# Kernel optimization log

Measured on AMD Instinct MI355X. Metric: run time of the kernel, lower is better.

The kernel has to match this reference:

```python
import jax, jax.numpy as jnp
import numpy as np

PERI_IDX = np.array([0, 1, 2, 3, 5, 6, 7, 8])  # non-center taps of the 3x3 window


def _extract_patches(x, stride, padding):
    # x: [B,C,H,W] -> patches [B,C,9,Hout,Wout], tap k = di*3+dj (row-major), matching F.unfold.
    B, C, H, W = x.shape
    Hout = (H + 2 * padding - 3) // stride + 1
    Wout = (W + 2 * padding - 3) // stride + 1
    xp = jnp.pad(x, ((0, 0), (0, 0), (padding, padding), (padding, padding)))
    taps = [xp[:, :, di:di + (Hout - 1) * stride + 1:stride, dj:dj + (Wout - 1) * stride + 1:stride]
            for di in range(3) for dj in range(3)]
    return jnp.stack(taps, axis=2)  # [B,C,9,Hout,Wout]


def setup_inputs() -> dict:
    key = jax.random.key(0)
    k1, k2, k3, k4 = jax.random.split(key, 4)
    B, C, O, H, W = 8, 64, 64, 128, 128
    x = jax.random.normal(k1, (B, C, H, W), dtype=jnp.float32)
    core = jax.random.normal(k2, (O, C, 1, 1), dtype=jnp.float32) * (1.0 / np.sqrt(C))
    periphery = jax.random.uniform(k3, (8,), dtype=jnp.float32, minval=-0.1, maxval=0.1)
    threshold = jnp.array([0.1], dtype=jnp.float32)
    scale = jnp.array([10.0], dtype=jnp.float32)
    return {"x": x, "core": core, "periphery": periphery, "threshold": threshold,
            "scale": scale, "stride": 1, "padding": 1}


def reference(x, core, periphery, threshold, scale, stride, padding):
    B, C, H, W = x.shape
    O = core.shape[0]
    patches = _extract_patches(x, stride, padding)           # [B,C,9,Ho,Wo]
    center = patches[:, :, 4]                                 # [B,C,Ho,Wo]
    # per-pixel variance-like routing statistic over channels and taps
    div = jnp.sum((patches - center[:, :, None]) ** 2, axis=(1, 2))  # [B,Ho,Wo]
    m_hard = jax.nn.sigmoid((div - threshold[0]) * scale[0]) > 0.5   # [B,Ho,Wo] bool
    w = core.reshape(O, C)
    # path 0 (low variance): 1x1 conv on the center pixel
    zero_out = jnp.einsum('bchw,oc->bohw', center, w)
    # path 1 (high variance): periphery-weighted sum then 1x1 conv
    agg = jnp.einsum('bckhw,k->bchw', patches[:, :, PERI_IDX], periphery)
    one_out = jnp.einsum('bchw,oc->bohw', agg, w)
    return jnp.where(m_hard[:, None], one_out, zero_out)
```

## Files before the change

### kernel.cpp

```cpp
#include <hip/hip_runtime.h>
#include <hip/hip_bf16.h>

constexpr int Bc = 8;
constexpr int Cc = 64;
constexpr int Oc = 64;
constexpr int Hc = 128;
constexpr int Wc = 128;
constexpr int HWc = Hc * Wc;
constexpr int CP = 72;

typedef __attribute__((ext_vector_type(8))) short short8;
typedef __attribute__((ext_vector_type(4))) float floatx4;

__global__ __launch_bounds__(512) void spconv_kernel(
    const float* __restrict__ x, const float* __restrict__ core,
    const float* __restrict__ peri, const float* __restrict__ thr,
    const float* __restrict__ scl, float* __restrict__ out)
{
    __shared__ __hip_bfloat16 s_selT[Wc][CP];
    __shared__ __hip_bfloat16 s_core[Oc][CP];
    __shared__ float s_divp[4][Wc];
    __shared__ float s_msk[Wc];

    const int tid = threadIdx.x;
    const int w   = tid & (Wc - 1);
    const int q   = tid >> 7;
    const int b   = blockIdx.x >> 7;
    const int h   = blockIdx.x & (Hc - 1);

    #pragma unroll
    for (int i = 0; i < 8; ++i) {
        const int idx = i * 512 + tid;
        s_core[idx >> 6][idx & 63] = __float2bfloat16(core[idx]);
    }

    const float* xb = x + (size_t)b * Cc * HWc + (size_t)h * Wc;

    const int   dh[8] = {-1,-1,-1, 0, 0, 1, 1, 1};
    const int   dw[8] = {-1, 0, 1,-1, 1,-1, 0, 1};
    int   off[8];
    float pl[8], mf[8];
    #pragma unroll
    for (int k = 0; k < 8; ++k) {
        const bool okh = (h + dh[k] >= 0) && (h + dh[k] < Hc);
        const bool okw = (w + dw[k] >= 0) && (w + dw[k] < Wc);
        const bool ok  = okh && okw;
        off[k] = ok ? (w + dh[k] * Wc + dw[k]) : w;
        mf[k]  = ok ? 1.f : 0.f;
        pl[k]  = ok ? peri[k] : 0.f;
    }

    float divacc = 0.f;
    const float* rowq = xb + (size_t)(q * 16) * HWc;
    #pragma unroll 4
    for (int ci = 0; ci < 16; ++ci) {
        const float* row = rowq + (size_t)ci * HWc;
        const float t4 = row[w];
        float v[8];
        #pragma unroll
        for (int k = 0; k < 8; ++k) v[k] = row[off[k]];
        float agg = 0.f;
        #pragma unroll
        for (int k = 0; k < 8; ++k) agg = fmaf(pl[k], v[k], agg);
        s_selT[w][q * 16 + ci] = __float2bfloat16(agg);
        #pragma unroll
        for (int k = 0; k < 8; ++k) {
            const float d = fmaf(mf[k], v[k], -t4);
            divacc = fmaf(d, d, divacc);
        }
    }
    s_divp[q][w] = divacc;
    __syncthreads();

    if (tid < Wc) {
        const float div = s_divp[0][tid] + s_divp[1][tid]
                        + s_divp[2][tid] + s_divp[3][tid];
        s_msk[tid] = (((div - thr[0]) * scl[0]) > 0.f) ? 1.f : 0.f;
    }
    __syncthreads();

    #pragma unroll
    for (int i = 0; i < 16; ++i) {
        const int idx = i * 512 + tid;
        const int ww  = idx & (Wc - 1);
        const int c   = idx >> 7;
        if (s_msk[ww] == 0.f)
            s_selT[ww][c] = __float2bfloat16(xb[(size_t)c * HWc + ww]);
    }
    __syncthreads();

    const int lane = tid & 63;
    const int wid  = tid >> 6;
    const int o0   = (wid & 3) * 16;
    const int wh   = wid >> 2;
    const int n    = lane & 15;
    const int quad = lane >> 4;

    const short8 a0 = *(const short8*)&s_core[o0 + n][quad * 8];
    const short8 a1 = *(const short8*)&s_core[o0 + n][quad * 8 + 32];

    float* outb = out + ((size_t)(b * Oc) * Hc + h) * Wc;

    #pragma unroll
    for (int t = 0; t < 4; ++t) {
        const int w0 = (wh * 4 + t) * 16;
        const short8 b0 = *(const short8*)&s_selT[w0 + n][quad * 8];
        const short8 b1 = *(const short8*)&s_selT[w0 + n][quad * 8 + 32];
        floatx4 acc = {0.f, 0.f, 0.f, 0.f};
        acc = __builtin_amdgcn_mfma_f32_16x16x32_bf16(a0, b0, acc, 0, 0, 0);
        acc = __builtin_amdgcn_mfma_f32_16x16x32_bf16(a1, b1, acc, 0, 0, 0);
        #pragma unroll
        for (int r = 0; r < 4; ++r) {
            const int o = o0 + quad * 4 + r;
            outb[(size_t)o * HWc + w0 + n] = acc[r];
        }
    }
}

extern "C" void kernel_launch(void* const* d_in, const int* in_sizes, int n_in,
                              void* d_out, int out_size, void* d_ws, size_t ws_size,
                              hipStream_t stream) {
    const float* x    = (const float*)d_in[0];
    const float* core = (const float*)d_in[1];
    const float* peri = (const float*)d_in[2];
    const float* thr  = (const float*)d_in[3];
    const float* scl  = (const float*)d_in[4];
    float* out = (float*)d_out;

    spconv_kernel<<<dim3(Bc * Hc), dim3(512), 0, stream>>>(
        x, core, peri, thr, scl, out);
}
```

Measured before the change: 106.4 us.

## Register-tile stencil with 4-wide pixel vectors and reorder blocks batch-inner

```diff
diff --git a/kernel.cpp b/kernel.cpp
--- a/kernel.cpp
+++ b/kernel.cpp
@@ -19,14 +19,13 @@
 {
     __shared__ __hip_bfloat16 s_selT[Wc][CP];
     __shared__ __hip_bfloat16 s_core[Oc][CP];
-    __shared__ float s_divp[4][Wc];
+    __shared__ float s_divp[16][132];
     __shared__ float s_msk[Wc];
 
     const int tid = threadIdx.x;
-    const int w   = tid & (Wc - 1);
-    const int q   = tid >> 7;
-    const int b   = blockIdx.x >> 7;
-    const int h   = blockIdx.x & (Hc - 1);
+    const int blk = blockIdx.x;
+    const int b   = blk & 7;
+    const int h   = blk >> 3;
 
     #pragma unroll
     for (int i = 0; i < 8; ++i) {
@@ -34,47 +33,81 @@
         s_core[idx >> 6][idx & 63] = __float2bfloat16(core[idx]);
     }
 
+    const int cg = tid & 15;
+    const int s  = tid >> 4;
+    const int w0 = s * 4;
+    const int c0 = cg * 4;
+
     const float* xb = x + (size_t)b * Cc * HWc + (size_t)h * Wc;
 
-    const int   dh[8] = {-1,-1,-1, 0, 0, 1, 1, 1};
-    const int   dw[8] = {-1, 0, 1,-1, 1,-1, 0, 1};
-    int   off[8];
-    float pl[8], mf[8];
+    const float mU = (h > 0)      ? 1.f : 0.f;
+    const float mD = (h < Hc - 1) ? 1.f : 0.f;
+    const int   dU = (h > 0)      ? -Wc : 0;
+    const int   dD = (h < Hc - 1) ?  Wc : 0;
+    const float mL = (s > 0)  ? 1.f : 0.f;
+    const float mR = (s < 31) ? 1.f : 0.f;
+    const int   oL = (s > 0)  ? (w0 - 1) : w0;
+    const int   oR = (s < 31) ? (w0 + 4) : (w0 + 3);
+    const float mUL = mU * mL, mUR = mU * mR;
+    const float mDL = mD * mL, mDR = mD * mR;
+
+    const float p0 = peri[0], p1 = peri[1], p2 = peri[2], p3 = peri[3];
+    const float p4 = peri[4], p5 = peri[5], p6 = peri[6], p7 = peri[7];
+
+    float dv[4] = {0.f, 0.f, 0.f, 0.f};
+
     #pragma unroll
-    for (int k = 0; k < 8; ++k) {
-        const bool okh = (h + dh[k] >= 0) && (h + dh[k] < Hc);
-        const bool okw = (w + dw[k] >= 0) && (w + dw[k] < Wc);
-        const bool ok  = okh && okw;
-        off[k] = ok ? (w + dh[k] * Wc + dw[k]) : w;
-        mf[k]  = ok ? 1.f : 0.f;
-        pl[k]  = ok ? peri[k] : 0.f;
-    }
+    for (int ci = 0; ci < 4; ++ci) {
+        const float* rc = xb + (size_t)(c0 + ci) * HWc;
+        const float* ru = rc + dU;
+        const float* rd = rc + dD;
 
-    float divacc = 0.f;
-    const float* rowq = xb + (size_t)(q * 16) * HWc;
-    #pragma unroll 4
-    for (int ci = 0; ci < 16; ++ci) {
-        const float* row = rowq + (size_t)ci * HWc;
-        const float t4 = row[w];
-        float v[8];
+        const floatx4 c4 = *(const floatx4*)(rc + w0);
+        const floatx4 u4 = *(const floatx4*)(ru + w0);
+        const floatx4 d4 = *(const floatx4*)(rd + w0);
+
+        float U[6]  = { ru[oL] * mUL, u4[0] * mU, u4[1] * mU,
+                        u4[2] * mU,   u4[3] * mU, ru[oR] * mUR };
+        float Cv[6] = { rc[oL] * mL,  c4[0], c4[1],
+                        c4[2],        c4[3], rc[oR] * mR };
+        float D[6]  = { rd[oL] * mDL, d4[0] * mD, d4[1] * mD,
+                        d4[2] * mD,   d4[3] * mD, rd[oR] * mDR };
+
         #pragma unroll
-        for (int k = 0; k < 8; ++k) v[k] = row[off[k]];
-        float agg = 0.f;
-        #pragma unroll
-        for (int k = 0; k < 8; ++k) agg = fmaf(pl[k], v[k], agg);
-        s_selT[w][q * 16 + ci] = __float2bfloat16(agg);
-        #pragma unroll
-        for (int k = 0; k < 8; ++k) {
-            const float d = fmaf(mf[k], v[k], -t4);
-            divacc = fmaf(d, d, divacc);
+        for (int j = 0; j < 4; ++j) {
+            const float t = Cv[j + 1];
+            float agg =      p0 * U[j];
+            agg = fmaf(p1, U[j + 1],  agg);
+            agg = fmaf(p2, U[j + 2],  agg);
+            agg = fmaf(p3, Cv[j],     agg);
+            agg = fmaf(p4, Cv[j + 2], agg);
+            agg = fmaf(p5, D[j],      agg);
+            agg = fmaf(p6, D[j + 1],  agg);
+            agg = fmaf(p7, D[j + 2],  agg);
+            s_selT[w0 + j][c0 + ci] = __float2bfloat16(agg);
+
+            float e, dd;
+            e = U[j] - t;      dd = e * e;
+            e = U[j + 1] - t;  dd = fmaf(e, e, dd);
+            e = U[j + 2] - t;  dd = fmaf(e, e, dd);
+            e = Cv[j] - t;     dd = fmaf(e, e, dd);
+            e = Cv[j + 2] - t; dd = fmaf(e, e, dd);
+            e = D[j] - t;      dd = fmaf(e, e, dd);
+            e = D[j + 1] - t;  dd = fmaf(e, e, dd);
+            e = D[j + 2] - t;  dd = fmaf(e, e, dd);
+            dv[j] += dd;
         }
     }
-    s_divp[q][w] = divacc;
+    {
+        floatx4 dvv = { dv[0], dv[1], dv[2], dv[3] };
+        *(floatx4*)&s_divp[cg][w0] = dvv;
+    }
     __syncthreads();
 
     if (tid < Wc) {
-        const float div = s_divp[0][tid] + s_divp[1][tid]
-                        + s_divp[2][tid] + s_divp[3][tid];
+        float div = 0.f;
+        #pragma unroll
+        for (int g = 0; g < 16; ++g) div += s_divp[g][tid];
         s_msk[tid] = (((div - thr[0]) * scl[0]) > 0.f) ? 1.f : 0.f;
     }
     __syncthreads();
@@ -103,16 +136,16 @@
 
     #pragma unroll
     for (int t = 0; t < 4; ++t) {
-        const int w0 = (wh * 4 + t) * 16;
-        const short8 b0 = *(const short8*)&s_selT[w0 + n][quad * 8];
-        const short8 b1 = *(const short8*)&s_selT[w0 + n][quad * 8 + 32];
+        const int wt0 = (wh * 4 + t) * 16;
+        const short8 b0 = *(const short8*)&s_selT[wt0 + n][quad * 8];
+        const short8 b1 = *(const short8*)&s_selT[wt0 + n][quad * 8 + 32];
         floatx4 acc = {0.f, 0.f, 0.f, 0.f};
         acc = __builtin_amdgcn_mfma_f32_16x16x32_bf16(a0, b0, acc, 0, 0, 0);
         acc = __builtin_amdgcn_mfma_f32_16x16x32_bf16(a1, b1, acc, 0, 0, 0);
         #pragma unroll
         for (int r = 0; r < 4; ++r) {
             const int o = o0 + quad * 4 + r;
-            outb[(size_t)o * HWc + w0 + n] = acc[r];
+            outb[(size_t)o * HWc + wt0 + n] = acc[r];
         }
     }
 }
```

New measurement: 126.1 us. 18.5% more time.

## Build MFMA operands directly in registers, dropping shared memory and block barriers

Applied to the files above, without the earlier changes.

```diff
diff --git a/kernel.cpp b/kernel.cpp
--- a/kernel.cpp
+++ b/kernel.cpp
@@ -7,112 +7,133 @@
 constexpr int Hc = 128;
 constexpr int Wc = 128;
 constexpr int HWc = Hc * Wc;
-constexpr int CP = 72;
 
 typedef __attribute__((ext_vector_type(8))) short short8;
 typedef __attribute__((ext_vector_type(4))) float floatx4;
+typedef __attribute__((ext_vector_type(2))) float floatx2;
+typedef __attribute__((ext_vector_type(4))) unsigned uintx4;
 
-__global__ __launch_bounds__(512) void spconv_kernel(
+__device__ __forceinline__ unsigned cvt_pk_bf16(float lo, float hi) {
+    unsigned r;
+    asm("v_cvt_pk_bf16_f32 %0, %1, %2" : "=v"(r) : "v"(lo), "v"(hi));
+    return r;
+}
+
+__global__ __launch_bounds__(256, 4) void spconv_kernel(
     const float* __restrict__ x, const float* __restrict__ core,
     const float* __restrict__ peri, const float* __restrict__ thr,
     const float* __restrict__ scl, float* __restrict__ out)
 {
-    __shared__ __hip_bfloat16 s_selT[Wc][CP];
-    __shared__ __hip_bfloat16 s_core[Oc][CP];
-    __shared__ float s_divp[4][Wc];
-    __shared__ float s_msk[Wc];
+    const int tid  = threadIdx.x;
+    const int l    = tid & 63;
+    const int wv   = tid >> 6;
+    const int b    = blockIdx.x & 7;
+    const int rh   = blockIdx.x >> 3;
+    const int h    = rh >> 1;
+    const int half = rh & 1;
+    const int n    = l & 15;
+    const int quad = l >> 4;
+    const int w0   = half * 64 + wv * 16;
+    const int wpix = w0 + n;
 
-    const int tid = threadIdx.x;
-    const int w   = tid & (Wc - 1);
-    const int q   = tid >> 7;
-    const int b   = blockIdx.x >> 7;
-    const int h   = blockIdx.x & (Hc - 1);
+    const int  w2 = wpix & ~1;
+    const bool ep = (wpix & 1) != 0;
+    const bool lm = wpix > 0;
+    const bool rm = wpix < Wc - 1;
+    const int  eoff = ep ? (rm ? wpix + 1 : wpix) : (lm ? wpix - 1 : 0);
 
+    const float mUf = (h > 0) ? 1.f : 0.f;
+    const float mDf = (h < Hc - 1) ? 1.f : 0.f;
+    const int   dU  = (h > 0) ? -Wc : 0;
+    const int   dD  = (h < Hc - 1) ? Wc : 0;
+
+    const float p0 = peri[0], p1 = peri[1], p2 = peri[2], p3 = peri[3];
+    const float p4 = peri[4], p5 = peri[5], p6 = peri[6], p7 = peri[7];
+    const float thrv = thr[0], sclv = scl[0];
+
+    const float* rp0 = x + (size_t)b * Cc * HWc + (size_t)h * Wc;
+
+    float dacc = 0.f;
+    unsigned aggPk[8], cenPk[8];
+
+#define PROCC(CIDX, AGGV, CENV) do {                                          \
+    const float* rp = rp0 + (size_t)(CIDX) * HWc;                             \
+    const floatx2 vU = *(const floatx2*)(rp + dU + w2);                       \
+    const floatx2 vC = *(const floatx2*)(rp + w2);                            \
+    const floatx2 vD = *(const floatx2*)(rp + dD + w2);                       \
+    const float eU = rp[dU + eoff];                                           \
+    const float eC = rp[eoff];                                                \
+    const float eD = rp[dD + eoff];                                           \
+    const float uL = (ep ? vU.x : (lm ? eU : 0.f)) * mUf;                     \
+    const float uC = (ep ? vU.y : vU.x) * mUf;                                \
+    const float uR = (ep ? (rm ? eU : 0.f) : vU.y) * mUf;                     \
+    const float cL =  ep ? vC.x : (lm ? eC : 0.f);                            \
+    const float t  =  ep ? vC.y : vC.x;                                       \
+    const float cR =  ep ? (rm ? eC : 0.f) : vC.y;                            \
+    const float dL = (ep ? vD.x : (lm ? eD : 0.f)) * mDf;                     \
+    const float dC = (ep ? vD.y : vD.x) * mDf;                                \
+    const float dR = (ep ? (rm ? eD : 0.f) : vD.y) * mDf;                     \
+    float a = p0 * uL; a = fmaf(p1, uC, a); a = fmaf(p2, uR, a);              \
+    a = fmaf(p3, cL, a); a = fmaf(p4, cR, a);                                 \
+    a = fmaf(p5, dL, a); a = fmaf(p6, dC, a); a = fmaf(p7, dR, a);            \
+    AGGV = a; CENV = t;                                                       \
+    float e;                                                                  \
+    e = uL - t; dacc = fmaf(e, e, dacc); e = uC - t; dacc = fmaf(e, e, dacc); \
+    e = uR - t; dacc = fmaf(e, e, dacc); e = cL - t; dacc = fmaf(e, e, dacc); \
+    e = cR - t; dacc = fmaf(e, e, dacc); e = dL - t; dacc = fmaf(e, e, dacc); \
+    e = dC - t; dacc = fmaf(e, e, dacc); e = dR - t; dacc = fmaf(e, e, dacc); \
+} while (0)
+
+    const int cb = quad * 8;
     #pragma unroll
-    for (int i = 0; i < 8; ++i) {
-        const int idx = i * 512 + tid;
-        s_core[idx >> 6][idx & 63] = __float2bfloat16(core[idx]);
+    for (int hf = 0; hf < 2; ++hf) {
+        const int cbase = hf * 32 + cb;
+        #pragma unroll
+        for (int jp = 0; jp < 4; ++jp) {
+            float a0, c0v, a1, c1v;
+            PROCC(cbase + 2 * jp,     a0, c0v);
+            PROCC(cbase + 2 * jp + 1, a1, c1v);
+            aggPk[hf * 4 + jp] = cvt_pk_bf16(a0, a1);
+            cenPk[hf * 4 + jp] = cvt_pk_bf16(c0v, c1v);
+        }
+    }
+#undef PROCC
+
+    dacc += __shfl_xor(dacc, 16);
+    dacc += __shfl_xor(dacc, 32);
+    const bool one = ((dacc - thrv) * sclv) > 0.f;
+
+    union { unsigned u[4]; short8 s; } B0, B1;
+    #pragma unroll
+    for (int i = 0; i < 4; ++i) {
+        B0.u[i] = one ? aggPk[i]     : cenPk[i];
+        B1.u[i] = one ? aggPk[i + 4] : cenPk[i + 4];
     }
 
-    const float* xb = x + (size_t)b * Cc * HWc + (size_t)h * Wc;
-
-    const int   dh[8] = {-1,-1,-1, 0, 0, 1, 1, 1};
-    const int   dw[8] = {-1, 0, 1,-1, 1,-1, 0, 1};
-    int   off[8];
-    float pl[8], mf[8];
+    union { unsigned u[4]; short8 s; } A0[4], A1[4];
     #pragma unroll
-    for (int k = 0; k < 8; ++k) {
-        const bool okh = (h + dh[k] >= 0) && (h + dh[k] < Hc);
-        const bool okw = (w + dw[k] >= 0) && (w + dw[k] < Wc);
-        const bool ok  = okh && okw;
-        off[k] = ok ? (w + dh[k] * Wc + dw[k]) : w;
-        mf[k]  = ok ? 1.f : 0.f;
-        pl[k]  = ok ? peri[k] : 0.f;
+    for (int ot = 0; ot < 4; ++ot) {
+        const float* ar = core + (size_t)(ot * 16 + n) * Cc + cb;
+        const floatx4 f0 = *(const floatx4*)(ar);
+        const floatx4 f1 = *(const floatx4*)(ar + 4);
+        const floatx4 f2 = *(const floatx4*)(ar + 32);
+        const floatx4 f3 = *(const floatx4*)(ar + 36);
+        A0[ot].u[0] = cvt_pk_bf16(f0.x, f0.y); A0[ot].u[1] = cvt_pk_bf16(f0.z, f0.w);
+        A0[ot].u[2] = cvt_pk_bf16(f1.x, f1.y); A0[ot].u[3] = cvt_pk_bf16(f1.z, f1.w);
+        A1[ot].u[0] = cvt_pk_bf16(f2.x, f2.y); A1[ot].u[1] = cvt_pk_bf16(f2.z, f2.w);
+        A1[ot].u[2] = cvt_pk_bf16(f3.x, f3.y); A1[ot].u[3] = cvt_pk_bf16(f3.z, f3.w);
     }
 
-    float divacc = 0.f;
-    const float* rowq = xb + (size_t)(q * 16) * HWc;
-    #pragma unroll 4
-    for (int ci = 0; ci < 16; ++ci) {
-        const float* row = rowq + (size_t)ci * HWc;
-        const float t4 = row[w];
-        float v[8];
-        #pragma unroll
-        for (int k = 0; k < 8; ++k) v[k] = row[off[k]];
-        float agg = 0.f;
-        #pragma unroll
-        for (int k = 0; k < 8; ++k) agg = fmaf(pl[k], v[k], agg);
-        s_selT[w][q * 16 + ci] = __float2bfloat16(agg);
-        #pragma unroll
-        for (int k = 0; k < 8; ++k) {
-            const float d = fmaf(mf[k], v[k], -t4);
-            divacc = fmaf(d, d, divacc);
-        }
-    }
-    s_divp[q][w] = divacc;
-    __syncthreads();
-
-    if (tid < Wc) {
-        const float div = s_divp[0][tid] + s_divp[1][tid]
-                        + s_divp[2][tid] + s_divp[3][tid];
-        s_msk[tid] = (((div - thr[0]) * scl[0]) > 0.f) ? 1.f : 0.f;
-    }
-    __syncthreads();
-
+    float* outb = out + (size_t)b * Oc * HWc + (size_t)h * Wc + wpix;
     #pragma unroll
-    for (int i = 0; i < 16; ++i) {
-        const int idx = i * 512 + tid;
-        const int ww  = idx & (Wc - 1);
-        const int c   = idx >> 7;
-        if (s_msk[ww] == 0.f)
-            s_selT[ww][c] = __float2bfloat16(xb[(size_t)c * HWc + ww]);
-    }
-    __syncthreads();
-
-    const int lane = tid & 63;
-    const int wid  = tid >> 6;
-    const int o0   = (wid & 3) * 16;
-    const int wh   = wid >> 2;
-    const int n    = lane & 15;
-    const int quad = lane >> 4;
-
-    const short8 a0 = *(const short8*)&s_core[o0 + n][quad * 8];
-    const short8 a1 = *(const short8*)&s_core[o0 + n][quad * 8 + 32];
-
-    float* outb = out + ((size_t)(b * Oc) * Hc + h) * Wc;
-
-    #pragma unroll
-    for (int t = 0; t < 4; ++t) {
-        const int w0 = (wh * 4 + t) * 16;
-        const short8 b0 = *(const short8*)&s_selT[w0 + n][quad * 8];
-        const short8 b1 = *(const short8*)&s_selT[w0 + n][quad * 8 + 32];
+    for (int ot = 0; ot < 4; ++ot) {
         floatx4 acc = {0.f, 0.f, 0.f, 0.f};
-        acc = __builtin_amdgcn_mfma_f32_16x16x32_bf16(a0, b0, acc, 0, 0, 0);
-        acc = __builtin_amdgcn_mfma_f32_16x16x32_bf16(a1, b1, acc, 0, 0, 0);
+        acc = __builtin_amdgcn_mfma_f32_16x16x32_bf16(A0[ot].s, B0.s, acc, 0, 0, 0);
+        acc = __builtin_amdgcn_mfma_f32_16x16x32_bf16(A1[ot].s, B1.s, acc, 0, 0, 0);
         #pragma unroll
         for (int r = 0; r < 4; ++r) {
-            const int o = o0 + quad * 4 + r;
-            outb[(size_t)o * HWc + w0 + n] = acc[r];
+            const int o = ot * 16 + quad * 4 + r;
+            outb[(size_t)o * HWc] = acc[r];
         }
     }
 }
@@ -127,6 +148,6 @@
     const float* scl  = (const float*)d_in[4];
     float* out = (float*)d_out;
 
-    spconv_kernel<<<dim3(Bc * Hc), dim3(512), 0, stream>>>(
+    spconv_kernel<<<dim3(Bc * Hc * 2), dim3(256), 0, stream>>>(
         x, core, peri, thr, scl, out);
 }
```

New measurement: 124.9 us. +17.5%, slower.
